# Kernel tuning notes

Measured on AMD Instinct MI355X. Metric: run time of the kernel, lower is better.

The kernel has to match this reference:

```python
import jax, jax.numpy as jnp
import numpy as np

EPS = 1e-08
SIGMA = 0.1
B = 1.0


def setup_inputs() -> dict:
    key = jax.random.key(0)
    k1, k2 = jax.random.split(key)
    N, C, H, W = 4, 256, 64, 64
    featureT = jax.random.normal(k1, (N, C, H, W), dtype=jnp.float32)
    featureI = jax.random.normal(k2, (N, C, H, W), dtype=jnp.float32)
    return {"featureT": featureT, "featureI": featureI}


def reference(featureT, featureI):
    N, C, H, W = featureT.shape
    # center both by target mean over (batch, spatial)
    meanT = featureT.mean(axis=(0, 2, 3), keepdims=True)
    fI = featureI - meanT
    fT = featureT - meanT
    # channel-wise L2 normalize
    fI = fI / (jnp.linalg.norm(fI, axis=1, keepdims=True) + EPS)
    fT = fT / (jnp.linalg.norm(fT, axis=1, keepdims=True) + EPS)
    # 1x1-patch conv2d == contraction over channels: sim[n, p, h, w]
    # where p indexes the flattened H*W spatial positions of the target.
    fT_flat = fT.reshape(N, C, H * W)  # [N, C, P]
    sim = jnp.einsum('nchw,ncp->nphw', fI, fT_flat)  # [N, P, H, W]
    raw_dist = (1.0 - sim) / 2.0
    # relative distances: divide by min over patch axis
    div = jnp.min(raw_dist, axis=1, keepdims=True)
    relative_dist = raw_dist / (div + EPS)
    # contextual similarity: exp-weight + sum-normalize over patch axis
    Wt = jnp.exp((B - relative_dist) / (SIGMA + EPS))
    W_sum = Wt.sum(axis=1, keepdims=True)
    CX = Wt / (W_sum + EPS)
    # max over spatial dims of featureI, mean over patches, -log, mean over batch
    CX = CX.max(axis=(2, 3))           # [N, P]
    CX = CX.mean(axis=1)               # [N]
    CX_loss = -jnp.log(CX + EPS)
    return jnp.mean(CX_loss)
```

## Files before the change

### kernel.cpp

```cpp
#include <hip/hip_runtime.h>
#include <cmath>


#define NB 4
#define CC 256
#define HW 4096
#define NQ0 8
#define NCS 16

static constexpr float kEPS = 1e-8f;
static constexpr float kSIG = 0.1f + 1e-8f;

typedef __attribute__((ext_vector_type(8)))  short short8;
typedef __attribute__((ext_vector_type(16))) float f32x16;

enum {
  OFF_MEAN = 0,
  OFF_CMAX = 256,
  OFF_WSUM = OFF_CMAX + NQ0*NB*HW,
  OFF_MAXP = OFF_WSUM + NQ0*NB*HW,
  OFF_MAXV = OFF_MAXP + NCS*NB*HW,
  OFF_GT   = OFF_MAXV + NB*HW,
  OFF_GI   = OFF_GT + NB*HW*CC/2,
  WS_FLOATS_FULL = OFF_GI + NB*HW*CC/2
};

__device__ __forceinline__ ushort cvt_bf16(float x) {
  unsigned u = __float_as_uint(x);
  unsigned r = (u + 0x7fffu + ((u >> 16) & 1u)) >> 16;
  return (ushort)r;
}

__device__ __forceinline__ void glds16(const ushort* g, ushort* l) {
  __builtin_amdgcn_global_load_lds(
      (const __attribute__((address_space(1))) unsigned*)g,
      (__attribute__((address_space(3))) unsigned*)l, 16, 0, 0);
}
__device__ __forceinline__ void s_bar()  { asm volatile("s_barrier" ::: "memory"); }
__device__ __forceinline__ void w_vm4()  { asm volatile("s_waitcnt vmcnt(4)" ::: "memory"); }
__device__ __forceinline__ void w_vm0()  { asm volatile("s_waitcnt vmcnt(0)" ::: "memory"); }
__device__ __forceinline__ void w_lgkm() { asm volatile("s_waitcnt lgkmcnt(0)" ::: "memory"); }

__device__ __forceinline__ float blockSum256(float v) {
  __shared__ float sh[4];
  const int lane = threadIdx.x & 63, wv = threadIdx.x >> 6;
  #pragma unroll
  for (int o = 32; o > 0; o >>= 1) v += __shfl_down(v, o, 64);
  __syncthreads();
  if (lane == 0) sh[wv] = v;
  __syncthreads();
  return sh[0] + sh[1] + sh[2] + sh[3];
}

__global__ __launch_bounds__(256) void k_mean9(const float* __restrict__ fT,
                                               float* __restrict__ ws) {
  const int c = blockIdx.x, t = threadIdx.x;
  float s = 0.f;
  for (int n = 0; n < NB; ++n) {
    const float* p = fT + (size_t)(n*CC + c)*HW;
    #pragma unroll
    for (int k = 0; k < 16; ++k) s += p[k*256 + t];
  }
  const float tot = blockSum256(s);
  if (t == 0) ws[OFF_MEAN + c] = tot * (1.0f/16384.0f);
}

__global__ __launch_bounds__(256) void k_prep9(const float* __restrict__ fT,
                                               const float* __restrict__ fI,
                                               float* __restrict__ ws) {
  __shared__ float stage[32][257];
  __shared__ float prt[8][32];
  __shared__ float sinv[32];
  const int t = threadIdx.x, l = t & 63;
  int bid = blockIdx.x;
  const int tensor = (bid >= 512); bid &= 511;
  const int n   = bid >> 7;
  const int r32 = bid & 127;
  const int p0  = r32 * 32;

  const float* __restrict__ src = tensor ? fI : fT;
  ushort* __restrict__ dst = (ushort*)(ws + (tensor ? OFF_GI : OFF_GT));
  const float* __restrict__ mean = ws + OFF_MEAN;

  const int pl = t & 31, cg = t >> 5;
  float acc = 0.f;
  #pragma unroll
  for (int i = 0; i < 32; ++i) {
    const int c = cg*32 + i;
    const float v = src[((size_t)(n*CC + c))*HW + p0 + pl] - mean[c];
    stage[pl][c] = v;
    acc += v*v;
  }
  prt[cg][pl] = acc;
  __syncthreads();
  if (t < 32) {
    float s = 0.f;
    #pragma unroll
    for (int g = 0; g < 8; ++g) s += prt[g][t];
    sinv[t] = 1.0f/(sqrtf(s) + kEPS);
  }
  __syncthreads();

  const int w = t >> 6, lhi = l >> 5, m = l & 31;
  const float iv = sinv[m];
  #pragma unroll
  for (int i = 0; i < 4; ++i) {
    const int kc = w*4 + i;
    const int cb = kc*16 + lhi*8;
    short8 o;
    #pragma unroll
    for (int j = 0; j < 8; ++j)
      ((ushort*)&o)[j] = cvt_bf16(stage[m][cb + j] * iv);
    *(short8*)(dst + (((size_t)(n*128 + r32)*16 + kc) << 9) + l*8) = o;
  }
}


__global__ __launch_bounds__(256, 2) void k_gA(
    const ushort* __restrict__ gA, const ushort* __restrict__ gB,
    float* __restrict__ ws)
{
  __shared__ ushort Ab[2][8192];
  __shared__ float red2[256];

  const int t = threadIdx.x;
  const int w = t >> 6, l = t & 63;
  const int ln31 = l & 31;

  const int L = blockIdx.x;
  const int xcd = L & 7, j = L >> 3;
  const int sid = xcd*8 + (j & 7);
  const int h   = j >> 3;
  const int n = sid >> 4;
  const int col0 = (sid & 15) * 256;

  const ushort* __restrict__ gAn = gA + (size_t)(n*128 + h*16)*8192;

  #pragma unroll
  for (int i = 0; i < 4; ++i)
    glds16(gAn + (size_t)(i*256 + t)*8, &Ab[0][(i*256 + t)*8]);
  #pragma unroll
  for (int i = 0; i < 4; ++i)
    glds16(gAn + 8192 + (size_t)(i*256 + t)*8, &Ab[1][(i*256 + t)*8]);

  short8 breg0[16], breg1[16];
  {
    const int RB0 = (col0 >> 5) + w;
    const int RB1 = (col0 >> 5) + 4 + w;
    #pragma unroll
    for (int kc = 0; kc < 16; ++kc) {
      breg0[kc] = *(const short8*)(gB + (((size_t)(n*128 + RB0)*16 + kc) << 9) + l*8);
      breg1[kc] = *(const short8*)(gB + (((size_t)(n*128 + RB1)*16 + kc) << 9) + l*8);
    }
  }

  float run0 = -3.0e38f, run1 = -3.0e38f;

  for (int iter = 0; iter < 16; ++iter) {
    if (iter < 15) w_vm4(); else w_vm0();
    s_bar();

    const ushort* __restrict__ Abuf = &Ab[iter & 1][0];
    f32x16 acc0, acc1;
    #pragma unroll
    for (int e = 0; e < 16; ++e) { acc0[e] = 0.f; acc1[e] = 0.f; }
    #pragma unroll
    for (int kc = 0; kc < 16; ++kc) {
      const short8 a0 = *(const short8*)&Abuf[kc*512 + l*8];
      acc0 = __builtin_amdgcn_mfma_f32_32x32x16_bf16(a0, breg0[kc], acc0, 0, 0, 0);
      acc1 = __builtin_amdgcn_mfma_f32_32x32x16_bf16(a0, breg1[kc], acc1, 0, 0, 0);
    }
    w_lgkm();
    s_bar();
    if (iter + 2 < 16) {
      const ushort* __restrict__ src = gAn + (size_t)(iter + 2)*8192;
      ushort* __restrict__ dstl = &Ab[iter & 1][0];
      #pragma unroll
      for (int i = 0; i < 4; ++i)
        glds16(src + (size_t)(i*256 + t)*8, dstl + (i*256 + t)*8);
    }

    #pragma unroll
    for (int r = 0; r < 16; ++r) {
      run0 = fmaxf(run0, acc0[r]);
      run1 = fmaxf(run1, acc1[r]);
    }
  }

  run0 = fmaxf(run0, __shfl_xor(run0, 32, 64));
  run1 = fmaxf(run1, __shfl_xor(run1, 32, 64));
  if (l < 32) {
    red2[w*32 + ln31]       = run0;
    red2[128 + w*32 + ln31] = run1;
  }
  __syncthreads();
  ws[OFF_CMAX + h*(NB*HW) + n*HW + col0 + t] = red2[t];
}

__global__ __launch_bounds__(256, 2) void k_gB(
    const ushort* __restrict__ gA, const ushort* __restrict__ gB,
    float* __restrict__ ws)
{
  __shared__ ushort Ab[2][8192];
  __shared__ float red2[256];

  const int t = threadIdx.x;
  const int w = t >> 6, l = t & 63;
  const int ln31 = l & 31;

  const int L = blockIdx.x;
  const int xcd = L & 7, j = L >> 3;
  const int sid = xcd*8 + (j & 7);
  const int h   = j >> 3;
  const int n = sid >> 4;
  const int col0 = (sid & 15) * 256;

  const ushort* __restrict__ gAn = gA + (size_t)(n*128 + h*16)*8192;

  #pragma unroll
  for (int i = 0; i < 4; ++i)
    glds16(gAn + (size_t)(i*256 + t)*8, &Ab[0][(i*256 + t)*8]);
  #pragma unroll
  for (int i = 0; i < 4; ++i)
    glds16(gAn + 8192 + (size_t)(i*256 + t)*8, &Ab[1][(i*256 + t)*8]);

  float aq0, bq0, aq1, bq1;
  {
    const int q0 = col0 + w*32 + ln31;
    const int q1 = q0 + 128;
    float cm0 = -3.0e38f, cm1 = -3.0e38f;
    #pragma unroll
    for (int hh = 0; hh < NQ0; ++hh) {
      cm0 = fmaxf(cm0, ws[OFF_CMAX + hh*(NB*HW) + n*HW + q0]);
      cm1 = fmaxf(cm1, ws[OFF_CMAX + hh*(NB*HW) + n*HW + q1]);
    }
    const float i0 = 1.0f/(2.0f*(0.5f*(1.0f - cm0) + kEPS));
    const float i1 = 1.0f/(2.0f*(0.5f*(1.0f - cm1) + kEPS));
    bq0 = i0 / kSIG; aq0 = (1.0f - i0) / kSIG;
    bq1 = i1 / kSIG; aq1 = (1.0f - i1) / kSIG;
  }

  short8 breg0[16], breg1[16];
  {
    const int RB0 = (col0 >> 5) + w;
    const int RB1 = (col0 >> 5) + 4 + w;
    #pragma unroll
    for (int kc = 0; kc < 16; ++kc) {
      breg0[kc] = *(const short8*)(gB + (((size_t)(n*128 + RB0)*16 + kc) << 9) + l*8);
      breg1[kc] = *(const short8*)(gB + (((size_t)(n*128 + RB1)*16 + kc) << 9) + l*8);
    }
  }

  float ws0 = 0.f, ws1 = 0.f;

  for (int iter = 0; iter < 16; ++iter) {
    if (iter < 15) w_vm4(); else w_vm0();
    s_bar();

    const ushort* __restrict__ Abuf = &Ab[iter & 1][0];
    f32x16 acc0, acc1;
    #pragma unroll
    for (int e = 0; e < 16; ++e) { acc0[e] = 0.f; acc1[e] = 0.f; }
    #pragma unroll
    for (int kc = 0; kc < 16; ++kc) {
      const short8 a0 = *(const short8*)&Abuf[kc*512 + l*8];
      acc0 = __builtin_amdgcn_mfma_f32_32x32x16_bf16(a0, breg0[kc], acc0, 0, 0, 0);
      acc1 = __builtin_amdgcn_mfma_f32_32x32x16_bf16(a0, breg1[kc], acc1, 0, 0, 0);
    }
    w_lgkm();
    s_bar();
    if (iter + 2 < 16) {
      const ushort* __restrict__ src = gAn + (size_t)(iter + 2)*8192;
      ushort* __restrict__ dstl = &Ab[iter & 1][0];
      #pragma unroll
      for (int i = 0; i < 4; ++i)
        glds16(src + (size_t)(i*256 + t)*8, dstl + (i*256 + t)*8);
    }

    #pragma unroll
    for (int r = 0; r < 16; ++r) {
      ws0 += __expf(fmaf(bq0, acc0[r], aq0));
      ws1 += __expf(fmaf(bq1, acc1[r], aq1));
    }
  }

  ws0 += __shfl_xor(ws0, 32, 64);
  ws1 += __shfl_xor(ws1, 32, 64);
  if (l < 32) {
    red2[w*32 + ln31]       = ws0;
    red2[128 + w*32 + ln31] = ws1;
  }
  __syncthreads();
  ws[OFF_WSUM + h*(NB*HW) + n*HW + col0 + t] = red2[t];
}

__global__ __launch_bounds__(256, 2) void k_gC(
    const ushort* __restrict__ gA, const ushort* __restrict__ gB,
    float* __restrict__ ws)
{
  __shared__ ushort Ab[2][8192];
  __shared__ float Ef[32*264];
  __shared__ float gam[256], bet[256];

  const int t = threadIdx.x;
  const int w = t >> 6, l = t & 63;
  const int ln31 = l & 31, lhi = l >> 5;

  const int L = blockIdx.x;
  const int xcd = L & 7, j = L >> 3;
  const int sid = xcd*8 + (j & 7);
  const int h   = j >> 3;
  const int n = sid >> 4;
  const int cs = sid & 15;
  const int col0 = cs * 256;

  {
    const int idx = n*HW + col0 + t;
    float cm = -3.0e38f;
    #pragma unroll
    for (int hh = 0; hh < NQ0; ++hh)
      cm = fmaxf(cm, ws[OFF_CMAX + hh*(NB*HW) + idx]);
    const float inv2d = 1.0f/(2.0f*(0.5f*(1.0f - cm) + kEPS));
    const float beta  = inv2d / kSIG;
    const float alpha = (1.0f - inv2d) / kSIG;
    float sw = 0.f;
    #pragma unroll
    for (int hh = 0; hh < NQ0; ++hh)
      sw += ws[OFF_WSUM + hh*(NB*HW) + idx];
    gam[t] = alpha - logf(sw + kEPS);
    bet[t] = beta;
  }
  __syncthreads();

  const float gq0 = gam[w*32 + ln31],       bq0 = bet[w*32 + ln31];
  const float gq1 = gam[128 + w*32 + ln31], bq1 = bet[128 + w*32 + ln31];

  const ushort* __restrict__ gAn = gA + (size_t)(n*128 + h*16)*8192;

  #pragma unroll
  for (int i = 0; i < 4; ++i)
    glds16(gAn + (size_t)(i*256 + t)*8, &Ab[0][(i*256 + t)*8]);
  #pragma unroll
  for (int i = 0; i < 4; ++i)
    glds16(gAn + 8192 + (size_t)(i*256 + t)*8, &Ab[1][(i*256 + t)*8]);

  short8 breg0[16], breg1[16];
  {
    const int RB0 = (col0 >> 5) + w;
    const int RB1 = (col0 >> 5) + 4 + w;
    #pragma unroll
    for (int kc = 0; kc < 16; ++kc) {
      breg0[kc] = *(const short8*)(gB + (((size_t)(n*128 + RB0)*16 + kc) << 9) + l*8);
      breg1[kc] = *(const short8*)(gB + (((size_t)(n*128 + RB1)*16 + kc) << 9) + l*8);
    }
  }

  const int ecol = w*32 + ln31;
  const int lr = t >> 3, qc = (t & 7) * 32;
  float* __restrict__ MAXP = ws + OFF_MAXP + (size_t)cs*(NB*HW) + n*HW;

  for (int iter = 0; iter < 16; ++iter) {
    if (iter < 15) w_vm4(); else w_vm0();
    w_lgkm();
    s_bar();

    const ushort* __restrict__ Abuf = &Ab[iter & 1][0];
    f32x16 acc0, acc1;
    #pragma unroll
    for (int e = 0; e < 16; ++e) { acc0[e] = 0.f; acc1[e] = 0.f; }
    #pragma unroll
    for (int kc = 0; kc < 16; ++kc) {
      const short8 a0 = *(const short8*)&Abuf[kc*512 + l*8];
      acc0 = __builtin_amdgcn_mfma_f32_32x32x16_bf16(a0, breg0[kc], acc0, 0, 0, 0);
      acc1 = __builtin_amdgcn_mfma_f32_32x32x16_bf16(a0, breg1[kc], acc1, 0, 0, 0);
    }

    #pragma unroll
    for (int r = 0; r < 16; ++r) {
      const int lrow = 4*lhi + (r & 3) + 8*(r >> 2);
      Ef[lrow*264 + ecol]       = fmaf(bq0, acc0[r], gq0);
      Ef[lrow*264 + 128 + ecol] = fmaf(bq1, acc1[r], gq1);
    }
    w_lgkm();
    s_bar();
    if (iter + 2 < 16) {
      const ushort* __restrict__ src = gAn + (size_t)(iter + 2)*8192;
      ushort* __restrict__ dstl = &Ab[iter & 1][0];
      #pragma unroll
      for (int i = 0; i < 4; ++i)
        glds16(src + (size_t)(i*256 + t)*8, dstl + (i*256 + t)*8);
    }

    float m = -3.0e38f;
    #pragma unroll
    for (int k4 = 0; k4 < 8; ++k4) {
      const float4 v = *(const float4*)&Ef[lr*264 + qc + 4*k4];
      m = fmaxf(m, fmaxf(fmaxf(v.x, v.y), fmaxf(v.z, v.w)));
    }
    m = fmaxf(m, __shfl_xor(m, 1, 64));
    m = fmaxf(m, __shfl_xor(m, 2, 64));
    m = fmaxf(m, __shfl_xor(m, 4, 64));
    if ((t & 7) == 0) MAXP[h*512 + iter*32 + lr] = m;
  }
}

__global__ __launch_bounds__(256) void k_red(float* __restrict__ ws) {
  const int idx = blockIdx.x*256 + threadIdx.x;
  float m = ws[OFF_MAXP + idx];
  #pragma unroll
  for (int cs = 1; cs < NCS; ++cs)
    m = fmaxf(m, ws[OFF_MAXP + cs*(NB*HW) + idx]);
  ws[OFF_MAXV + idx] = m;
}

__global__ __launch_bounds__(256) void k_final9(const float* __restrict__ ws,
                                                float* __restrict__ out) {
  const int t = threadIdx.x;
  float loss = 0.f;
  for (int n = 0; n < NB; ++n) {
    float s = 0.f;
    for (int k = 0; k < 16; ++k)
      s += __expf(ws[OFF_MAXV + n*HW + k*256 + t]);
    const float tot = blockSum256(s);
    loss += -logf(tot*(1.0f/4096.0f) + kEPS);
  }
  if (t == 0) out[0] = loss*0.25f;
}

extern "C" void kernel_launch(void* const* d_in, const int* in_sizes, int n_in,
                              void* d_out, int out_size, void* d_ws, size_t ws_size,
                              hipStream_t stream) {
  const float* fT = (const float*)d_in[0];
  const float* fI = (const float*)d_in[1];
  float* out = (float*)d_out;
  float* ws  = (float*)d_ws;

  const size_t need_full = (size_t)WS_FLOATS_FULL * sizeof(float);
  if (ws_size < need_full) return;

  const ushort* GT = (const ushort*)(ws + OFF_GT);
  const ushort* GI = (const ushort*)(ws + OFF_GI);
  k_mean9 <<<256,  256, 0, stream>>>(fT, ws);
  k_prep9 <<<1024, 256, 0, stream>>>(fT, fI, ws);
  k_gA    <<<512,  256, 0, stream>>>(GT, GI, ws);
  k_gB    <<<512,  256, 0, stream>>>(GT, GI, ws);
  k_gC    <<<512,  256, 0, stream>>>(GT, GI, ws);
  k_red   <<<64,   256, 0, stream>>>(ws);
  k_final9<<<1,    256, 0, stream>>>(ws, out);
}
```

Before: 182.4 us.

## Swap MFMA operands in k_gC to reduce row max in registers and remap blocks

k_gC now issues the MFMA with the B and A operands swapped, so each lane's accumulator entries run along the reduction axis. The per-row max over columns can then be taken in registers with one cross-half shuffle instead of staging a 32x264 float tile in LDS and reading it back. Per-wave partial maxima go into a small stash and are combined once after the loop, which removes a barrier and LDS traffic from every iteration. The block-to-(n,h,cs) mapping across XCDs is also changed in all three GEMM kernels so that blocks sharing an A slab sit on the same XCD, and the A prefetch is issued before the gamma/beta setup. The cost is extra LDS reads of gamma and beta inside the loop.

```diff
diff --git a/kernel.cpp b/kernel.cpp
--- a/kernel.cpp
+++ b/kernel.cpp
@@ -128,13 +128,13 @@
   const int ln31 = l & 31;
 
   const int L = blockIdx.x;
-  const int xcd = L & 7, j = L >> 3;
-  const int sid = xcd*8 + (j & 7);
-  const int h   = j >> 3;
-  const int n = sid >> 4;
-  const int col0 = (sid & 15) * 256;
-
-  const ushort* __restrict__ gAn = gA + (size_t)(n*128 + h*16)*8192;
+  const int xcd = L & 7, g = L >> 3;
+  const int nh = xcd*4 + (g & 3);
+  const int cs = g >> 2;
+  const int n = nh >> 3, h = nh & 7;
+  const int col0 = cs * 256;
+
+  const ushort* __restrict__ gAn = gA + ((size_t)(n*128 + h*16) << 13);
 
   #pragma unroll
   for (int i = 0; i < 4; ++i)
@@ -145,8 +145,7 @@
 
   short8 breg0[16], breg1[16];
   {
-    const int RB0 = (col0 >> 5) + w;
-    const int RB1 = (col0 >> 5) + 4 + w;
+    const int RB0 = cs*8 + w, RB1 = cs*8 + 4 + w;
     #pragma unroll
     for (int kc = 0; kc < 16; ++kc) {
       breg0[kc] = *(const short8*)(gB + (((size_t)(n*128 + RB0)*16 + kc) << 9) + l*8);
@@ -209,13 +208,13 @@
   const int ln31 = l & 31;
 
   const int L = blockIdx.x;
-  const int xcd = L & 7, j = L >> 3;
-  const int sid = xcd*8 + (j & 7);
-  const int h   = j >> 3;
-  const int n = sid >> 4;
-  const int col0 = (sid & 15) * 256;
-
-  const ushort* __restrict__ gAn = gA + (size_t)(n*128 + h*16)*8192;
+  const int xcd = L & 7, g = L >> 3;
+  const int nh = xcd*4 + (g & 3);
+  const int cs = g >> 2;
+  const int n = nh >> 3, h = nh & 7;
+  const int col0 = cs * 256;
+
+  const ushort* __restrict__ gAn = gA + ((size_t)(n*128 + h*16) << 13);
 
   #pragma unroll
   for (int i = 0; i < 4; ++i)
@@ -242,8 +241,7 @@
 
   short8 breg0[16], breg1[16];
   {
-    const int RB0 = (col0 >> 5) + w;
-    const int RB1 = (col0 >> 5) + 4 + w;
+    const int RB0 = cs*8 + w, RB1 = cs*8 + 4 + w;
     #pragma unroll
     for (int kc = 0; kc < 16; ++kc) {
       breg0[kc] = *(const short8*)(gB + (((size_t)(n*128 + RB0)*16 + kc) << 9) + l*8);
@@ -299,20 +297,28 @@
     float* __restrict__ ws)
 {
   __shared__ ushort Ab[2][8192];
-  __shared__ float Ef[32*264];
-  __shared__ float gam[256], bet[256];
+  __shared__ float gam_s[256], bet_s[256];
+  __shared__ float stash[4][512];
 
   const int t = threadIdx.x;
   const int w = t >> 6, l = t & 63;
   const int ln31 = l & 31, lhi = l >> 5;
 
   const int L = blockIdx.x;
-  const int xcd = L & 7, j = L >> 3;
-  const int sid = xcd*8 + (j & 7);
-  const int h   = j >> 3;
-  const int n = sid >> 4;
-  const int cs = sid & 15;
+  const int xcd = L & 7, g = L >> 3;
+  const int nh = xcd*4 + (g & 3);
+  const int cs = g >> 2;
+  const int n = nh >> 3, h = nh & 7;
   const int col0 = cs * 256;
+
+  const ushort* __restrict__ gAn = gA + ((size_t)(n*128 + h*16) << 13);
+
+  #pragma unroll
+  for (int i = 0; i < 4; ++i)
+    glds16(gAn + (size_t)(i*256 + t)*8, &Ab[0][(i*256 + t)*8]);
+  #pragma unroll
+  for (int i = 0; i < 4; ++i)
+    glds16(gAn + 8192 + (size_t)(i*256 + t)*8, &Ab[1][(i*256 + t)*8]);
 
   {
     const int idx = n*HW + col0 + t;
@@ -320,66 +326,39 @@
     #pragma unroll
     for (int hh = 0; hh < NQ0; ++hh)
       cm = fmaxf(cm, ws[OFF_CMAX + hh*(NB*HW) + idx]);
-    const float inv2d = 1.0f/(2.0f*(0.5f*(1.0f - cm) + kEPS));
-    const float beta  = inv2d / kSIG;
-    const float alpha = (1.0f - inv2d) / kSIG;
     float sw = 0.f;
     #pragma unroll
     for (int hh = 0; hh < NQ0; ++hh)
       sw += ws[OFF_WSUM + hh*(NB*HW) + idx];
-    gam[t] = alpha - logf(sw + kEPS);
-    bet[t] = beta;
-  }
-  __syncthreads();
-
-  const float gq0 = gam[w*32 + ln31],       bq0 = bet[w*32 + ln31];
-  const float gq1 = gam[128 + w*32 + ln31], bq1 = bet[128 + w*32 + ln31];
-
-  const ushort* __restrict__ gAn = gA + (size_t)(n*128 + h*16)*8192;
-
-  #pragma unroll
-  for (int i = 0; i < 4; ++i)
-    glds16(gAn + (size_t)(i*256 + t)*8, &Ab[0][(i*256 + t)*8]);
-  #pragma unroll
-  for (int i = 0; i < 4; ++i)
-    glds16(gAn + 8192 + (size_t)(i*256 + t)*8, &Ab[1][(i*256 + t)*8]);
+    const float i0 = 1.0f/(2.0f*(0.5f*(1.0f - cm) + kEPS));
+    bet_s[t] = i0 / kSIG;
+    gam_s[t] = (1.0f - i0) / kSIG - logf(sw + kEPS);
+  }
 
   short8 breg0[16], breg1[16];
   {
-    const int RB0 = (col0 >> 5) + w;
-    const int RB1 = (col0 >> 5) + 4 + w;
+    const int RB0 = cs*8 + w, RB1 = cs*8 + 4 + w;
     #pragma unroll
     for (int kc = 0; kc < 16; ++kc) {
       breg0[kc] = *(const short8*)(gB + (((size_t)(n*128 + RB0)*16 + kc) << 9) + l*8);
       breg1[kc] = *(const short8*)(gB + (((size_t)(n*128 + RB1)*16 + kc) << 9) + l*8);
     }
   }
-
-  const int ecol = w*32 + ln31;
-  const int lr = t >> 3, qc = (t & 7) * 32;
-  float* __restrict__ MAXP = ws + OFF_MAXP + (size_t)cs*(NB*HW) + n*HW;
+  __syncthreads();
 
   for (int iter = 0; iter < 16; ++iter) {
     if (iter < 15) w_vm4(); else w_vm0();
-    w_lgkm();
     s_bar();
 
     const ushort* __restrict__ Abuf = &Ab[iter & 1][0];
-    f32x16 acc0, acc1;
-    #pragma unroll
-    for (int e = 0; e < 16; ++e) { acc0[e] = 0.f; acc1[e] = 0.f; }
+    f32x16 accq0, accq1;
+    #pragma unroll
+    for (int e = 0; e < 16; ++e) { accq0[e] = 0.f; accq1[e] = 0.f; }
     #pragma unroll
     for (int kc = 0; kc < 16; ++kc) {
       const short8 a0 = *(const short8*)&Abuf[kc*512 + l*8];
-      acc0 = __builtin_amdgcn_mfma_f32_32x32x16_bf16(a0, breg0[kc], acc0, 0, 0, 0);
-      acc1 = __builtin_amdgcn_mfma_f32_32x32x16_bf16(a0, breg1[kc], acc1, 0, 0, 0);
-    }
-
-    #pragma unroll
-    for (int r = 0; r < 16; ++r) {
-      const int lrow = 4*lhi + (r & 3) + 8*(r >> 2);
-      Ef[lrow*264 + ecol]       = fmaf(bq0, acc0[r], gq0);
-      Ef[lrow*264 + 128 + ecol] = fmaf(bq1, acc1[r], gq1);
+      accq0 = __builtin_amdgcn_mfma_f32_32x32x16_bf16(breg0[kc], a0, accq0, 0, 0, 0);
+      accq1 = __builtin_amdgcn_mfma_f32_32x32x16_bf16(breg1[kc], a0, accq1, 0, 0, 0);
     }
     w_lgkm();
     s_bar();
@@ -393,14 +372,23 @@
 
     float m = -3.0e38f;
     #pragma unroll
-    for (int k4 = 0; k4 < 8; ++k4) {
-      const float4 v = *(const float4*)&Ef[lr*264 + qc + 4*k4];
-      m = fmaxf(m, fmaxf(fmaxf(v.x, v.y), fmaxf(v.z, v.w)));
-    }
-    m = fmaxf(m, __shfl_xor(m, 1, 64));
-    m = fmaxf(m, __shfl_xor(m, 2, 64));
-    m = fmaxf(m, __shfl_xor(m, 4, 64));
-    if ((t & 7) == 0) MAXP[h*512 + iter*32 + lr] = m;
+    for (int r = 0; r < 16; ++r) {
+      const int row = (r & 3) + 8*(r >> 2) + 4*lhi;
+      const float g0v = gam_s[w*32 + row],       b0v = bet_s[w*32 + row];
+      const float g1v = gam_s[128 + w*32 + row], b1v = bet_s[128 + w*32 + row];
+      m = fmaxf(m, fmaf(b0v, accq0[r], g0v));
+      m = fmaxf(m, fmaf(b1v, accq1[r], g1v));
+    }
+    m = fmaxf(m, __shfl_xor(m, 32, 64));
+    if (l < 32) stash[w][iter*32 + ln31] = m;
+  }
+
+  __syncthreads();
+  float* __restrict__ MAXP = ws + OFF_MAXP + (size_t)cs*(NB*HW) + n*HW + h*512;
+  #pragma unroll
+  for (int p = t; p < 512; p += 256) {
+    MAXP[p] = fmaxf(fmaxf(stash[0][p], stash[1][p]),
+                    fmaxf(stash[2][p], stash[3][p]));
   }
 }
 
@@ -408,8 +396,8 @@
   const int idx = blockIdx.x*256 + threadIdx.x;
   float m = ws[OFF_MAXP + idx];
   #pragma unroll
-  for (int cs = 1; cs < NCS; ++cs)
-    m = fmaxf(m, ws[OFF_MAXP + cs*(NB*HW) + idx]);
+  for (int s = 1; s < NCS; ++s)
+    m = fmaxf(m, ws[OFF_MAXP + s*(NB*HW) + idx]);
   ws[OFF_MAXV + idx] = m;
 }
 
```

New measurement: 174.8 us (median of 2 runs). 4.1% less time.
